# Optimization experiments

Measured on AMD Instinct MI355X. Metric: run time of the kernel, lower is better.

## Reference

```python
import jax, jax.numpy as jnp
import numpy as np

B, NL2, NRC, NIN = 32768, 4, 8, 41
NCTRL = NIN + NL2 + NIN  # 86


def _blur(n):
    # tridiagonal blur: 0.8 on diag, 0.1 on the two off-diagonals (symmetric)
    return 0.8 * jnp.eye(n, dtype=jnp.float32) \
         + 0.1 * jnp.eye(n, k=1, dtype=jnp.float32) \
         + 0.1 * jnp.eye(n, k=-1, dtype=jnp.float32)


def _leaky(x):
    return jnp.where(x >= 0, x, 0.2 * x)  # LeakyReLU(0.2)


def _passgate(w, b, rc, x):
    # w: [B,out,in,rc] clamped to [-1,1]; rc: [B,rc]; x: [B,in] -> [B,out]
    w2 = jnp.einsum('boir,br->boi', jnp.clip(w, -1.0, 1.0), rc)
    return jnp.einsum('boi,bi->bo', w2, x) + b


def setup_inputs() -> dict:
    key = jax.random.key(0)
    ks = jax.random.split(key, 4)
    s_f = np.float32(np.sqrt(2.0 / (NIN * NRC)))
    s_r = np.float32(np.sqrt(2.0 / (NL2 * NRC)))
    inp = jax.random.normal(ks[0], (B, NIN), dtype=jnp.float32)
    fpg_w = jnp.clip(jax.random.normal(ks[1], (B, NL2, NIN, NRC), dtype=jnp.float32) * s_f, -1.0, 1.0)
    rpg_w = jnp.clip(jax.random.normal(ks[2], (B, NIN, NL2, NRC), dtype=jnp.float32) * s_r, -1.0, 1.0)
    fpg_b = jnp.zeros((B, NL2), dtype=jnp.float32)
    rpg_b = jnp.zeros((B, NIN), dtype=jnp.float32)
    # pgctrl: shared nn.Linear(86, 8) (default torch init ~ U(-1/sqrt(86), 1/sqrt(86)))
    bound = np.float32(1.0 / np.sqrt(NCTRL))
    kw, kb = jax.random.split(ks[3])
    pgctrl_w = jax.random.uniform(kw, (NRC, NCTRL), dtype=jnp.float32, minval=-bound, maxval=bound)
    pgctrl_b = jax.random.uniform(kb, (NRC,), dtype=jnp.float32, minval=-bound, maxval=bound)
    return {"inp": inp, "fpg_w": fpg_w, "fpg_b": fpg_b,
            "rpg_w": rpg_w, "rpg_b": rpg_b,
            "pgctrl_w": pgctrl_w, "pgctrl_b": pgctrl_b}


def reference(inp, fpg_w, fpg_b, rpg_w, rpg_b, pgctrl_w, pgctrl_b):
    rcblur = _blur(NRC)   # [8,8]
    l2blur = _blur(NL2)   # [4,4]
    # initial state buffers are zeros; note l2old/rcold are NOT updated inside
    # the outer loop (faithful to the original), only l1i carries over.
    l2old = jnp.zeros((B, NL2), dtype=inp.dtype)
    rcold = jnp.zeros((B, NRC), dtype=inp.dtype)
    l1i = jnp.zeros((B, NIN), dtype=inp.dtype)
    l2 = l2old
    rc = rcold
    for _ in range(2):
        rcin = jnp.concatenate([inp, l2old, inp - l1i], axis=1)  # [B,86]
        rc = _leaky(rcin @ pgctrl_w.T + pgctrl_b)
        rc = jnp.clip(0.4 * rc + 0.6 * rcold, -0.2, 1.0)
        for _ in range(3):
            rc = rc @ rcblur.T
        l2 = _passgate(fpg_w, fpg_b, rc, inp) * 0.1 + 0.9 * l2old
        l2 = jnp.clip(l2, -0.2, 1.0)
        for _ in range(2):
            l2 = l2 @ l2blur.T
        l1i = jnp.clip(_passgate(rpg_w, rpg_b, rc, l2), -0.2, 1.0)
    return (l1i, l2, rc)
```

## Files before the change

### kernel.cpp

```cpp
#include <hip/hip_runtime.h>

#define B_ROWS 32768
#define NIN 41
#define NL2 4
#define NRC 8

__device__ __forceinline__ float med3(float v, float lo, float hi) {
    return __builtin_amdgcn_fmed3f(v, lo, hi);
}

__device__ __forceinline__ float rl63(float v) {
    return __int_as_float(__builtin_amdgcn_readlane(__float_as_int(v), 63));
}

#define DPP8(C) \
    "v_add_f32_dpp %0, %0, %0 " C " row_mask:0xf bank_mask:0xf bound_ctrl:0\n\t" \
    "v_add_f32_dpp %1, %1, %1 " C " row_mask:0xf bank_mask:0xf bound_ctrl:0\n\t" \
    "v_add_f32_dpp %2, %2, %2 " C " row_mask:0xf bank_mask:0xf bound_ctrl:0\n\t" \
    "v_add_f32_dpp %3, %3, %3 " C " row_mask:0xf bank_mask:0xf bound_ctrl:0\n\t" \
    "v_add_f32_dpp %4, %4, %4 " C " row_mask:0xf bank_mask:0xf bound_ctrl:0\n\t" \
    "v_add_f32_dpp %5, %5, %5 " C " row_mask:0xf bank_mask:0xf bound_ctrl:0\n\t" \
    "v_add_f32_dpp %6, %6, %6 " C " row_mask:0xf bank_mask:0xf bound_ctrl:0\n\t" \
    "v_add_f32_dpp %7, %7, %7 " C " row_mask:0xf bank_mask:0xf bound_ctrl:0\n\t"

__device__ __forceinline__ void wave_sum8(float* v) {
    asm("s_nop 1\n\t"
        DPP8("row_shr:1")
        DPP8("row_shr:2")
        DPP8("row_shr:4")
        DPP8("row_shr:8")
        DPP8("row_bcast:15")
        DPP8("row_bcast:31")
        "s_nop 1"
        : "+v"(v[0]), "+v"(v[1]), "+v"(v[2]), "+v"(v[3]),
          "+v"(v[4]), "+v"(v[5]), "+v"(v[6]), "+v"(v[7]));
}

#define DPP4(C) \
    "v_add_f32_dpp %0, %0, %0 " C " row_mask:0xf bank_mask:0xf bound_ctrl:0\n\t" \
    "v_add_f32_dpp %1, %1, %1 " C " row_mask:0xf bank_mask:0xf bound_ctrl:0\n\t" \
    "v_add_f32_dpp %2, %2, %2 " C " row_mask:0xf bank_mask:0xf bound_ctrl:0\n\t" \
    "v_add_f32_dpp %3, %3, %3 " C " row_mask:0xf bank_mask:0xf bound_ctrl:0\n\t"

__device__ __forceinline__ void wave_sum4(float* v) {
    asm("s_nop 1\n\t"
        DPP4("row_shr:1")
        DPP4("row_shr:2")
        DPP4("row_shr:4")
        DPP4("row_shr:8")
        DPP4("row_bcast:15")
        DPP4("row_bcast:31")
        "s_nop 1"
        : "+v"(v[0]), "+v"(v[1]), "+v"(v[2]), "+v"(v[3]));
}

__device__ __forceinline__ void blur8(float* v) {
    float t[NRC];
    #pragma unroll
    for (int r = 0; r < NRC; ++r) {
        float s = 0.8f * v[r];
        if (r > 0)       s += 0.1f * v[r - 1];
        if (r < NRC - 1) s += 0.1f * v[r + 1];
        t[r] = s;
    }
    #pragma unroll
    for (int r = 0; r < NRC; ++r) v[r] = t[r];
}

__device__ __forceinline__ void blur4(float* v) {
    float t[NL2];
    #pragma unroll
    for (int o = 0; o < NL2; ++o) {
        float s = 0.8f * v[o];
        if (o > 0)       s += 0.1f * v[o - 1];
        if (o < NL2 - 1) s += 0.1f * v[o + 1];
        t[o] = s;
    }
    #pragma unroll
    for (int o = 0; o < NL2; ++o) v[o] = t[o];
}

__global__ void __launch_bounds__(256, 4) pgnet_kernel(
    const float* __restrict__ inp,
    const float* __restrict__ fpg_w,
    const float* __restrict__ fpg_b,
    const float* __restrict__ rpg_w,
    const float* __restrict__ rpg_b,
    const float* __restrict__ pgw,
    const float* __restrict__ pgb,
    float* __restrict__ out)
{
    const int lane = threadIdx.x & 63;
    const int row  = blockIdx.x * 4 + (threadIdx.x >> 6);
    const bool act = lane < NIN;
    const int safe = act ? lane : (NIN - 1);


    float w1r[NRC], w2r[NRC];
    #pragma unroll
    for (int r = 0; r < NRC; ++r) {
        w1r[r] = pgw[r * 86 + safe];
        w2r[r] = pgw[r * 86 + 45 + safe];
    }
    const float x_raw = inp[row * NIN + safe];
    const float4 fbv  = *(const float4*)(fpg_b + (size_t)row * NL2);
    const float  rb_r = rpg_b[row * NIN + safe];
    __builtin_amdgcn_sched_barrier(0);

    const float* fp = fpg_w + (size_t)row * 1312 + (size_t)safe * 8;
    float4 fwv[NL2][2];
    #pragma unroll
    for (int o = 0; o < NL2; ++o) {
        fwv[o][0] = *(const float4*)(fp + o * 328);
        fwv[o][1] = *(const float4*)(fp + o * 328 + 4);
    }
    __builtin_amdgcn_sched_barrier(0);

    const float* rp = rpg_w + (size_t)row * 1312 + (size_t)safe * 32;
    float4 rwv[8];
    #pragma unroll
    for (int j = 0; j < 8; ++j) rwv[j] = ((const float4*)rp)[j];
    __builtin_amdgcn_sched_barrier(0);

    const float x  = act ? x_raw : 0.0f;
    const float rb = act ? rb_r  : 0.0f;

    float t8[NRC];
    #pragma unroll
    for (int r = 0; r < NRC; ++r) t8[r] = x * (w1r[r] + w2r[r]);
    wave_sum8(t8);
    float A[NRC], W2[NRC];
    #pragma unroll
    for (int r = 0; r < NRC; ++r) {
        A[r]  = rl63(t8[r]) + pgb[r];
        W2[r] = act ? w2r[r] : 0.0f;
    }

    const float fb[NL2] = {fbv.x, fbv.y, fbv.z, fbv.w};

    float l1, rcv[NRC], l2v[NL2];

    #pragma unroll
    for (int r = 0; r < NRC; ++r) {
        const float pre = A[r];
        const float v = (pre >= 0.f) ? pre : 0.2f * pre;
        rcv[r] = med3(0.4f * v, -0.2f, 1.0f);
    }
    blur8(rcv); blur8(rcv); blur8(rcv);

    float fw[NL2][NRC];
    #pragma unroll
    for (int o = 0; o < NL2; ++o) {
        fw[o][0] = med3(fwv[o][0].x, -1.f, 1.f); fw[o][1] = med3(fwv[o][0].y, -1.f, 1.f);
        fw[o][2] = med3(fwv[o][0].z, -1.f, 1.f); fw[o][3] = med3(fwv[o][0].w, -1.f, 1.f);
        fw[o][4] = med3(fwv[o][1].x, -1.f, 1.f); fw[o][5] = med3(fwv[o][1].y, -1.f, 1.f);
        fw[o][6] = med3(fwv[o][1].z, -1.f, 1.f); fw[o][7] = med3(fwv[o][1].w, -1.f, 1.f);
    }

    float t4[NL2];
    #pragma unroll
    for (int o = 0; o < NL2; ++o) {
        float d = 0.f;
        #pragma unroll
        for (int r = 0; r < NRC; ++r) d += fw[o][r] * rcv[r];
        t4[o] = x * d;
    }
    wave_sum4(t4);
    #pragma unroll
    for (int o = 0; o < NL2; ++o)
        l2v[o] = med3(0.1f * (rl63(t4[o]) + fb[o]), -0.2f, 1.0f);
    blur4(l2v); blur4(l2v);

    float rw[NL2][NRC];
    #pragma unroll
    for (int o = 0; o < NL2; ++o) {
        rw[o][0] = med3(rwv[2*o].x, -1.f, 1.f);   rw[o][1] = med3(rwv[2*o].y, -1.f, 1.f);
        rw[o][2] = med3(rwv[2*o].z, -1.f, 1.f);   rw[o][3] = med3(rwv[2*o].w, -1.f, 1.f);
        rw[o][4] = med3(rwv[2*o+1].x, -1.f, 1.f); rw[o][5] = med3(rwv[2*o+1].y, -1.f, 1.f);
        rw[o][6] = med3(rwv[2*o+1].z, -1.f, 1.f); rw[o][7] = med3(rwv[2*o+1].w, -1.f, 1.f);
    }

    {
        float acc = rb;
        #pragma unroll
        for (int o = 0; o < NL2; ++o) {
            float d = 0.f;
            #pragma unroll
            for (int r = 0; r < NRC; ++r) d += rw[o][r] * rcv[r];
            acc += l2v[o] * d;
        }
        l1 = med3(acc, -0.2f, 1.0f);
    }

    #pragma unroll
    for (int r = 0; r < NRC; ++r) t8[r] = l1 * W2[r];
    wave_sum8(t8);
    #pragma unroll
    for (int r = 0; r < NRC; ++r) {
        const float pre = A[r] - rl63(t8[r]);
        const float v = (pre >= 0.f) ? pre : 0.2f * pre;
        rcv[r] = med3(0.4f * v, -0.2f, 1.0f);
    }
    blur8(rcv); blur8(rcv); blur8(rcv);

    #pragma unroll
    for (int o = 0; o < NL2; ++o) {
        float d = 0.f;
        #pragma unroll
        for (int r = 0; r < NRC; ++r) d += fw[o][r] * rcv[r];
        t4[o] = x * d;
    }
    wave_sum4(t4);
    #pragma unroll
    for (int o = 0; o < NL2; ++o)
        l2v[o] = med3(0.1f * (rl63(t4[o]) + fb[o]), -0.2f, 1.0f);
    blur4(l2v); blur4(l2v);

    {
        float acc = rb;
        #pragma unroll
        for (int o = 0; o < NL2; ++o) {
            float d = 0.f;
            #pragma unroll
            for (int r = 0; r < NRC; ++r) d += rw[o][r] * rcv[r];
            acc += l2v[o] * d;
        }
        l1 = med3(acc, -0.2f, 1.0f);
    }

    if (act) out[(size_t)row * NIN + lane] = l1;
    if (lane < NL2) {
        float v = l2v[0];
        #pragma unroll
        for (int o = 1; o < NL2; ++o) if (lane == o) v = l2v[o];
        out[(size_t)B_ROWS * NIN + (size_t)row * NL2 + lane] = v;
    }
    if (lane < NRC) {
        float v = rcv[0];
        #pragma unroll
        for (int r = 1; r < NRC; ++r) if (lane == r) v = rcv[r];
        out[(size_t)B_ROWS * (NIN + NL2) + (size_t)row * NRC + lane] = v;
    }
}

extern "C" void kernel_launch(void* const* d_in, const int* in_sizes, int n_in,
                              void* d_out, int out_size, void* d_ws, size_t ws_size,
                              hipStream_t stream) {
    const float* inp   = (const float*)d_in[0];
    const float* fpg_w = (const float*)d_in[1];
    const float* fpg_b = (const float*)d_in[2];
    const float* rpg_w = (const float*)d_in[3];
    const float* rpg_b = (const float*)d_in[4];
    const float* pgw   = (const float*)d_in[5];
    const float* pgb   = (const float*)d_in[6];
    float* out = (float*)d_out;

    dim3 grid(B_ROWS / 4);
    dim3 block(256);
    hipLaunchKernelGGL(pgnet_kernel, grid, block, 0, stream,
                       inp, fpg_w, fpg_b, rpg_w, rpg_b, pgw, pgb, out);
}
```

Measured before the change: 359.5 us.

## Stage rpg weights into LDS via global_load_lds with XOR swizzle

Replaces the per-lane register load of the 32 rpg weights with direct global-to-LDS async copies (global_load_lds), XOR-swizzled to avoid bank conflicts, read back from LDS in each passgate. It also folds the two pgctrl weight halves into one register array, reloads the w2 half later, and raises launch bounds occupancy from 4 to 6. The goal is lower register pressure and more waves in flight to hide the memory-bound weight stream, at the cost of LDS traffic and about 21KB shared memory per block.

```diff
diff --git a/kernel.cpp b/kernel.cpp
--- a/kernel.cpp
+++ b/kernel.cpp
@@ -4,6 +4,7 @@
 #define NIN 41
 #define NL2 4
 #define NRC 8
+#define ROW_F 1344
 
 __device__ __forceinline__ float med3(float v, float lo, float hi) {
     return __builtin_amdgcn_fmed3f(v, lo, hi);
@@ -11,6 +12,13 @@
 
 __device__ __forceinline__ float rl63(float v) {
     return __int_as_float(__builtin_amdgcn_readlane(__float_as_int(v), 63));
+}
+
+__device__ __forceinline__ void stage16(const float* g, float* l) {
+    __builtin_amdgcn_global_load_lds(
+        (const __attribute__((address_space(1))) void*)g,
+        (__attribute__((address_space(3))) void*)l,
+        16, 0, 0);
 }
 
 #define DPP8(C) \
@@ -80,7 +88,7 @@
     for (int o = 0; o < NL2; ++o) v[o] = t[o];
 }
 
-__global__ void __launch_bounds__(256, 4) pgnet_kernel(
+__global__ void __launch_bounds__(256, 6) pgnet_kernel(
     const float* __restrict__ inp,
     const float* __restrict__ fpg_w,
     const float* __restrict__ fpg_b,
@@ -90,18 +98,18 @@
     const float* __restrict__ pgb,
     float* __restrict__ out)
 {
+    __shared__ __align__(16) float lds_rw[4][ROW_F];
+
     const int lane = threadIdx.x & 63;
-    const int row  = blockIdx.x * 4 + (threadIdx.x >> 6);
+    const int w    = threadIdx.x >> 6;
+    const int row  = blockIdx.x * 4 + w;
     const bool act = lane < NIN;
     const int safe = act ? lane : (NIN - 1);
 
-
-    float w1r[NRC], w2r[NRC];
-    #pragma unroll
-    for (int r = 0; r < NRC; ++r) {
-        w1r[r] = pgw[r * 86 + safe];
-        w2r[r] = pgw[r * 86 + 45 + safe];
-    }
+    float ws[NRC];
+    #pragma unroll
+    for (int r = 0; r < NRC; ++r)
+        ws[r] = pgw[r * 86 + safe] + pgw[r * 86 + 45 + safe];
     const float x_raw = inp[row * NIN + safe];
     const float4 fbv  = *(const float4*)(fpg_b + (size_t)row * NL2);
     const float  rb_r = rpg_b[row * NIN + safe];
@@ -116,10 +124,18 @@
     }
     __builtin_amdgcn_sched_barrier(0);
 
-    const float* rp = rpg_w + (size_t)row * 1312 + (size_t)safe * 32;
-    float4 rwv[8];
-    #pragma unroll
-    for (int j = 0; j < 8; ++j) rwv[j] = ((const float4*)rp)[j];
+    const float* rbase = rpg_w + (size_t)row * 1312;
+    float* lbase = &lds_rw[w][0];
+    #pragma unroll
+    for (int k = 0; k < 5; ++k) {
+        const int d = k * 64 + lane;
+        const int i = d >> 3;
+        const int j = (d & 7) ^ (i & 7);
+        stage16(rbase + i * 32 + j * 4, lbase + k * 256);
+    }
+    if (lane < 8) {
+        stage16(rbase + 40 * 32 + lane * 4, lbase + 5 * 256);
+    }
     __builtin_amdgcn_sched_barrier(0);
 
     const float x  = act ? x_raw : 0.0f;
@@ -127,14 +143,11 @@
 
     float t8[NRC];
     #pragma unroll
-    for (int r = 0; r < NRC; ++r) t8[r] = x * (w1r[r] + w2r[r]);
+    for (int r = 0; r < NRC; ++r) t8[r] = x * ws[r];
     wave_sum8(t8);
-    float A[NRC], W2[NRC];
-    #pragma unroll
-    for (int r = 0; r < NRC; ++r) {
-        A[r]  = rl63(t8[r]) + pgb[r];
-        W2[r] = act ? w2r[r] : 0.0f;
-    }
+    float A[NRC];
+    #pragma unroll
+    for (int r = 0; r < NRC; ++r) A[r] = rl63(t8[r]) + pgb[r];
 
     const float fb[NL2] = {fbv.x, fbv.y, fbv.z, fbv.w};
 
@@ -171,33 +184,40 @@
         l2v[o] = med3(0.1f * (rl63(t4[o]) + fb[o]), -0.2f, 1.0f);
     blur4(l2v); blur4(l2v);
 
-    float rw[NL2][NRC];
-    #pragma unroll
-    for (int o = 0; o < NL2; ++o) {
-        rw[o][0] = med3(rwv[2*o].x, -1.f, 1.f);   rw[o][1] = med3(rwv[2*o].y, -1.f, 1.f);
-        rw[o][2] = med3(rwv[2*o].z, -1.f, 1.f);   rw[o][3] = med3(rwv[2*o].w, -1.f, 1.f);
-        rw[o][4] = med3(rwv[2*o+1].x, -1.f, 1.f); rw[o][5] = med3(rwv[2*o+1].y, -1.f, 1.f);
-        rw[o][6] = med3(rwv[2*o+1].z, -1.f, 1.f); rw[o][7] = med3(rwv[2*o+1].w, -1.f, 1.f);
-    }
-
+    asm volatile("s_waitcnt vmcnt(0)" ::: "memory");
+    const float4* lrow = (const float4*)lbase;
+    const int swz = safe & 7;
     {
         float acc = rb;
         #pragma unroll
         for (int o = 0; o < NL2; ++o) {
+            const float4 a = lrow[safe * 8 + ((2 * o)     ^ swz)];
+            const float4 b = lrow[safe * 8 + ((2 * o + 1) ^ swz)];
             float d = 0.f;
-            #pragma unroll
-            for (int r = 0; r < NRC; ++r) d += rw[o][r] * rcv[r];
+            d += med3(a.x, -1.f, 1.f) * rcv[0];
+            d += med3(a.y, -1.f, 1.f) * rcv[1];
+            d += med3(a.z, -1.f, 1.f) * rcv[2];
+            d += med3(a.w, -1.f, 1.f) * rcv[3];
+            d += med3(b.x, -1.f, 1.f) * rcv[4];
+            d += med3(b.y, -1.f, 1.f) * rcv[5];
+            d += med3(b.z, -1.f, 1.f) * rcv[6];
+            d += med3(b.w, -1.f, 1.f) * rcv[7];
             acc += l2v[o] * d;
         }
         l1 = med3(acc, -0.2f, 1.0f);
     }
 
-    #pragma unroll
-    for (int r = 0; r < NRC; ++r) t8[r] = l1 * W2[r];
-    wave_sum8(t8);
-    #pragma unroll
-    for (int r = 0; r < NRC; ++r) {
-        const float pre = A[r] - rl63(t8[r]);
+    __builtin_amdgcn_sched_barrier(0);
+    float corr[NRC];
+    #pragma unroll
+    for (int r = 0; r < NRC; ++r) {
+        const float w2 = pgw[r * 86 + 45 + safe];
+        corr[r] = act ? (l1 * w2) : 0.0f;
+    }
+    wave_sum8(corr);
+    #pragma unroll
+    for (int r = 0; r < NRC; ++r) {
+        const float pre = A[r] - rl63(corr[r]);
         const float v = (pre >= 0.f) ? pre : 0.2f * pre;
         rcv[r] = med3(0.4f * v, -0.2f, 1.0f);
     }
@@ -220,9 +240,17 @@
         float acc = rb;
         #pragma unroll
         for (int o = 0; o < NL2; ++o) {
+            const float4 a = lrow[safe * 8 + ((2 * o)     ^ swz)];
+            const float4 b = lrow[safe * 8 + ((2 * o + 1) ^ swz)];
             float d = 0.f;
-            #pragma unroll
-            for (int r = 0; r < NRC; ++r) d += rw[o][r] * rcv[r];
+            d += med3(a.x, -1.f, 1.f) * rcv[0];
+            d += med3(a.y, -1.f, 1.f) * rcv[1];
+            d += med3(a.z, -1.f, 1.f) * rcv[2];
+            d += med3(a.w, -1.f, 1.f) * rcv[3];
+            d += med3(b.x, -1.f, 1.f) * rcv[4];
+            d += med3(b.y, -1.f, 1.f) * rcv[5];
+            d += med3(b.z, -1.f, 1.f) * rcv[6];
+            d += med3(b.w, -1.f, 1.f) * rcv[7];
             acc += l2v[o] * d;
         }
         l1 = med3(acc, -0.2f, 1.0f);
```

Measured after the change: 395.0 us. 9.9% more time.
